# Kernel optimization log

Measured on AMD Instinct MI355X. Metric: run time of the kernel, lower is better.

## Reference

```python
import jax, jax.numpy as jnp
import numpy as np

V_CNT = 10000
B = 16
N = B * V_CNT          # total nodes
K = 6                  # Chebyshev order
CH = [3, 128, 64, 32, 128]
G = 8                  # GroupNorm groups (divides 128, 64, 32)
EPS = 1e-5
AVG_DEG = 16


def setup_inputs() -> dict:
    key = jax.random.key(0)
    ks = jax.random.split(key, 8)
    n_edges = N * AVG_DEG
    inp = {
        "x": jax.random.normal(ks[0], (N, CH[0]), jnp.float32),
        "edge_index": jax.random.randint(ks[1], (2, n_edges), 0, N, jnp.int32).astype(jnp.int64),
    }
    for l in range(3):
        cin, cout = CH[l], CH[l + 1]
        s = (1.0 / (cin * K)) ** 0.5
        inp[f"W{l}"] = jax.random.uniform(ks[2 + l], (K, cin, cout), jnp.float32, -s, s)
        inp[f"b{l}"] = jnp.zeros((cout,), jnp.float32)
        inp[f"gamma{l}"] = jnp.ones((cout,), jnp.float32)
        inp[f"beta{l}"] = jnp.zeros((cout,), jnp.float32)
    din = V_CNT * CH[3]
    s = (1.0 / din) ** 0.5
    inp["W_last"] = jax.random.uniform(ks[5], (din, CH[4]), jnp.float32, -s, s)
    inp["b_last"] = jnp.zeros((CH[4],), jnp.float32)
    return inp


def _cheb_edge_weights(edge_index):
    # PyG ChebConv sym normalization with lambda_max=2: L_hat = L - I = -D^{-1/2} A D^{-1/2}
    row, col = edge_index[0], edge_index[1]
    deg = jax.ops.segment_sum(jnp.ones(row.shape, jnp.float32), row, num_segments=N)
    dis = jnp.where(deg > 0, jax.lax.rsqrt(jnp.maximum(deg, 1.0)), 0.0)  # deg^{-1/2}, inf->0
    return -dis[row] * dis[col], row, col


def _cheb_conv(x, row, col, w, W, b):
    # Chebyshev recursion: Tx0=x, Tx1=L_hat x, Tx_k = 2 L_hat Tx_{k-1} - Tx_{k-2}
    prop = lambda h: jax.ops.segment_sum(w[:, None] * h[col], row, num_segments=N)
    Tx0 = x
    out = Tx0 @ W[0]
    Tx1 = prop(Tx0)
    out = out + Tx1 @ W[1]
    for k in range(2, W.shape[0]):
        Tx2 = 2.0 * prop(Tx1) - Tx0
        out = out + Tx2 @ W[k]
        Tx0, Tx1 = Tx1, Tx2
    return out + b


def _group_norm(h, gamma, beta):
    n, C = h.shape
    hg = h.reshape(n, G, C // G)
    mu = hg.mean(axis=2, keepdims=True)
    var = hg.var(axis=2, keepdims=True)
    hg = (hg - mu) * jax.lax.rsqrt(var + EPS)
    return hg.reshape(n, C) * gamma + beta


def reference(x, edge_index, W0, b0, gamma0, beta0, W1, b1, gamma1, beta1,
              W2, b2, gamma2, beta2, W_last, b_last):
    w, row, col = _cheb_edge_weights(edge_index)
    Ws = [W0, W1, W2]
    bs = [b0, b1, b2]
    gs = [gamma0, gamma1, gamma2]
    betas = [beta0, beta1, beta2]
    h = x
    for l in range(3):
        h = _cheb_conv(h, row, col, w, Ws[l], bs[l])
        h = _group_norm(h, gs[l], betas[l])
        h = jax.nn.relu(h)
    h = h.reshape(-1, V_CNT * CH[3])  # [B, v_cnt*32]
    return h @ W_last + b_last
```

## Files before the change

### kernel.cpp

```cpp
#include <hip/hip_runtime.h>
#include <hip/hip_fp16.h>


#define NN 160000
#define EE 2560000
#define FD2 256

typedef __attribute__((ext_vector_type(8))) _Float16 half8;
typedef __attribute__((ext_vector_type(4))) float floatx4;

__device__ inline float2 h2f2(unsigned u) {
  __half2 h = __builtin_bit_cast(__half2, u);
  return __half22float2(h);
}
__device__ inline unsigned short f2h(float f) {
  return __builtin_bit_cast(unsigned short, __float2half_rn(f));
}
__device__ inline unsigned packh2(float a, float b) {
  return __builtin_bit_cast(unsigned, __floats2half2_rn(a, b));
}

__global__ __launch_bounds__(256) void k_zero(int* __restrict__ p, int n) {
  int i = blockIdx.x * 256 + threadIdx.x;
  if (i < n) p[i] = 0;
}

__global__ __launch_bounds__(256) void k_hist(const int* __restrict__ ei, int* __restrict__ deg) {
  int e = blockIdx.x * 256 + threadIdx.x;
  if (e < EE) atomicAdd(&deg[ei[e]], 1);
}

__global__ __launch_bounds__(256) void k_dis(const int* __restrict__ deg, float* __restrict__ dis) {
  int i = blockIdx.x * 256 + threadIdx.x;
  if (i < NN) { int d = deg[i]; dis[i] = d > 0 ? rsqrtf((float)d) : 0.f; }
}

__global__ __launch_bounds__(256) void k_scan1(const int* __restrict__ deg, int* __restrict__ rowStart,
                                               int* __restrict__ bsum) {
  __shared__ int s[256];
  int tid = threadIdx.x;
  int i = blockIdx.x * 256 + tid;
  int v = deg[i];
  s[tid] = v;
  __syncthreads();
  for (int off = 1; off < 256; off <<= 1) {
    int t = (tid >= off) ? s[tid - off] : 0;
    __syncthreads();
    s[tid] += t;
    __syncthreads();
  }
  rowStart[i] = s[tid] - v;
  if (tid == 255) bsum[blockIdx.x] = s[255];
}

__global__ void k_scan2(int* __restrict__ bsum, int nb) {
  __shared__ int s[1024];
  int tid = threadIdx.x;
  int v = (tid < nb) ? bsum[tid] : 0;
  s[tid] = v;
  __syncthreads();
  for (int off = 1; off < 1024; off <<= 1) {
    int t = (tid >= off) ? s[tid - off] : 0;
    __syncthreads();
    s[tid] += t;
    __syncthreads();
  }
  if (tid < nb) bsum[tid] = s[tid] - v;
}

__global__ __launch_bounds__(256) void k_scan3(int* __restrict__ rowStart, const int* __restrict__ bsum) {
  int i = blockIdx.x * 256 + threadIdx.x;
  rowStart[i] += bsum[blockIdx.x];
  if (i == 0) rowStart[NN] = EE;
}

__global__ __launch_bounds__(256) void k_scatter(const int* __restrict__ ei, const int* __restrict__ rowStart,
                                                 int* __restrict__ cursor, const float* __restrict__ dis,
                                                 int2* __restrict__ ew) {
  int e = blockIdx.x * 256 + threadIdx.x;
  if (e >= EE) return;
  int r = ei[e];
  int c = ei[EE + e];
  int pos = rowStart[r] + atomicAdd(&cursor[r], 1);
  ew[pos] = make_int2(c, __float_as_int(-dis[r] * dis[c]));
}

__global__ __launch_bounds__(256) void k_copyx(const float* __restrict__ x, float* __restrict__ A,
                                               unsigned short* __restrict__ TxAll) {
  int i = blockIdx.x * 256 + threadIdx.x;
  if (i < NN * 3) {
    float v = x[i];
    A[i] = v;
    int node = i / 3, c = i - node * 3;
    TxAll[node * 32 + c] = f2h(v);
  }
}

template <int MODE>
__global__ __launch_bounds__(256) void k_prop3(const float* __restrict__ Tsrc, float* __restrict__ Tdst,
                                               unsigned short* __restrict__ TxAll, int ks,
                                               const int* __restrict__ rowStart, const int2* __restrict__ ew) {
  int i = blockIdx.x * 256 + threadIdx.x;
  if (i >= NN) return;
  float a0 = 0.f, a1 = 0.f, a2 = 0.f;
  int e = rowStart[i], e1 = rowStart[i + 1];
  for (; e + 3 < e1; e += 4) {
    int2 p0 = ew[e], p1 = ew[e + 1], p2 = ew[e + 2], p3 = ew[e + 3];
    float w0 = __int_as_float(p0.y), w1 = __int_as_float(p1.y);
    float w2 = __int_as_float(p2.y), w3 = __int_as_float(p3.y);
    a0 += w0 * Tsrc[p0.x * 3] + w1 * Tsrc[p1.x * 3] + w2 * Tsrc[p2.x * 3] + w3 * Tsrc[p3.x * 3];
    a1 += w0 * Tsrc[p0.x * 3 + 1] + w1 * Tsrc[p1.x * 3 + 1] + w2 * Tsrc[p2.x * 3 + 1] + w3 * Tsrc[p3.x * 3 + 1];
    a2 += w0 * Tsrc[p0.x * 3 + 2] + w1 * Tsrc[p1.x * 3 + 2] + w2 * Tsrc[p2.x * 3 + 2] + w3 * Tsrc[p3.x * 3 + 2];
  }
  for (; e < e1; e++) {
    int2 p0 = ew[e];
    float w0 = __int_as_float(p0.y);
    a0 += w0 * Tsrc[p0.x * 3];
    a1 += w0 * Tsrc[p0.x * 3 + 1];
    a2 += w0 * Tsrc[p0.x * 3 + 2];
  }
  if (MODE == 2) {
    a0 = 2.f * a0 - Tdst[i * 3];
    a1 = 2.f * a1 - Tdst[i * 3 + 1];
    a2 = 2.f * a2 - Tdst[i * 3 + 2];
  }
  Tdst[i * 3] = a0; Tdst[i * 3 + 1] = a1; Tdst[i * 3 + 2] = a2;
  unsigned short* tp = TxAll + i * 32 + ks * 3;
  tp[0] = f2h(a0); tp[1] = f2h(a1); tp[2] = f2h(a2);
}

__global__ __launch_bounds__(256) void k_padW0(const float* __restrict__ W0, unsigned short* __restrict__ Bt) {
  int idx = blockIdx.x * 256 + threadIdx.x;
  if (idx >= 128 * 32) return;
  int co = idx >> 5, t = idx & 31;
  Bt[co * 32 + t] = (t < 18) ? f2h(W0[t * 128 + co]) : (unsigned short)0;
}

template <int CIN, int COUT>
__global__ __launch_bounds__(256) void k_combine(const float* __restrict__ W, unsigned short* __restrict__ Bt) {
  int idx = blockIdx.x * 256 + threadIdx.x;
  if (idx >= CIN * 6 * COUT) return;
  int co = idx % COUT;
  int j  = (idx / COUT) % 6;
  int ci = idx / (6 * COUT);
  float c0, c1, c2, c3, c4, c5;
  switch (j) {
    case 0:  c0 = 1;  c1 = 0;  c2 = -1; c3 = 0;   c4 = 1;  c5 = 0;   break;
    case 1:  c0 = 0;  c1 = 1;  c2 = 0;  c3 = -3;  c4 = 0;  c5 = 5;   break;
    case 2:  c0 = 0;  c1 = 0;  c2 = 2;  c3 = 0;   c4 = -8; c5 = 0;   break;
    case 3:  c0 = 0;  c1 = 0;  c2 = 0;  c3 = 4;   c4 = 0;  c5 = -20; break;
    case 4:  c0 = 0;  c1 = 0;  c2 = 0;  c3 = 0;   c4 = 8;  c5 = 0;   break;
    default: c0 = 0;  c1 = 0;  c2 = 0;  c3 = 0;   c4 = 0;  c5 = 16;  break;
  }
  float s = 0.f;
  s += c0 * W[(0 * CIN + ci) * COUT + co];
  s += c1 * W[(1 * CIN + ci) * COUT + co];
  s += c2 * W[(2 * CIN + ci) * COUT + co];
  s += c3 * W[(3 * CIN + ci) * COUT + co];
  s += c4 * W[(4 * CIN + ci) * COUT + co];
  s += c5 * W[(5 * CIN + ci) * COUT + co];
  Bt[(j * COUT + co) * CIN + ci] = f2h(s);
}

template <int KDIM, int COUT>
__global__ __launch_bounds__(256) void k_gemm(const unsigned short* __restrict__ A,
                                              const unsigned short* __restrict__ Bt,
                                              unsigned short* __restrict__ Y) {
  constexpr int KP = KDIM + 8;
  __shared__ unsigned short As[64 * KP];
  __shared__ unsigned short Bs[64 * KP];
  int i0 = blockIdx.x * 64;
  int c0 = blockIdx.y * 64;
  for (int idx = threadIdx.x; idx < 64 * (KDIM / 8); idx += 256) {
    int row = idx / (KDIM / 8), seg = idx % (KDIM / 8);
    uint4 v = ((const uint4*)A)[(size_t)(i0 + row) * (KDIM / 8) + seg];
    *reinterpret_cast<uint4*>(&As[row * KP + seg * 8]) = v;
  }
  for (int idx = threadIdx.x; idx < 64 * (KDIM / 8); idx += 256) {
    int row = idx / (KDIM / 8), seg = idx % (KDIM / 8);
    uint4 v = ((const uint4*)Bt)[(size_t)(c0 + row) * (KDIM / 8) + seg];
    *reinterpret_cast<uint4*>(&Bs[row * KP + seg * 8]) = v;
  }
  __syncthreads();
  int w = threadIdx.x >> 6, lane = threadIdx.x & 63;
  int mn = lane & 15, q = lane >> 4;
  floatx4 acc[4];
#pragma unroll
  for (int cb = 0; cb < 4; cb++) acc[cb] = {0.f, 0.f, 0.f, 0.f};
#pragma unroll
  for (int ks = 0; ks < KDIM / 32; ks++) {
    half8 af = *reinterpret_cast<const half8*>(&As[(16 * w + mn) * KP + ks * 32 + q * 8]);
#pragma unroll
    for (int cb = 0; cb < 4; cb++) {
      half8 bf = *reinterpret_cast<const half8*>(&Bs[(cb * 16 + mn) * KP + ks * 32 + q * 8]);
      acc[cb] = __builtin_amdgcn_mfma_f32_16x16x32_f16(af, bf, acc[cb], 0, 0, 0);
    }
  }
#pragma unroll
  for (int cb = 0; cb < 4; cb++) {
    int jc = c0 + cb * 16 + mn;
    int slice = jc / COUT, cc = jc % COUT;
    unsigned short* dst = Y + (size_t)slice * NN * COUT + cc;
#pragma unroll
    for (int r = 0; r < 4; r++) {
      int i = i0 + 16 * w + q * 4 + r;
      dst[(size_t)i * COUT] = f2h(acc[cb][r]);
    }
  }
}

template <int CPN>
__global__ __launch_bounds__(256) void k_horner(const unsigned* __restrict__ Ysrc, unsigned* __restrict__ Ydst,
                                                const int* __restrict__ rowStart, const int2* __restrict__ ew) {
  int t = blockIdx.x * 256 + threadIdx.x;
  int i = t / CPN;
  int cp = t % CPN;
  float2 a = h2f2(Ydst[(size_t)i * CPN + cp]);
  float acc0 = a.x, acc1 = a.y;
  int e = rowStart[i], e1 = rowStart[i + 1];
  for (; e + 7 < e1; e += 8) {
    int2 p[8];
    unsigned u[8];
#pragma unroll
    for (int k = 0; k < 8; k++) p[k] = ew[e + k];
#pragma unroll
    for (int k = 0; k < 8; k++) u[k] = Ysrc[(size_t)p[k].x * CPN + cp];
#pragma unroll
    for (int k = 0; k < 8; k++) {
      float w = __int_as_float(p[k].y);
      float2 f = h2f2(u[k]);
      acc0 += w * f.x;
      acc1 += w * f.y;
    }
  }
  for (; e < e1; e++) {
    int2 p0 = ew[e];
    float w0 = __int_as_float(p0.y);
    float2 f0 = h2f2(Ysrc[(size_t)p0.x * CPN + cp]);
    acc0 += w0 * f0.x;
    acc1 += w0 * f0.y;
  }
  Ydst[(size_t)i * CPN + cp] = packh2(acc0, acc1);
}

template <int CPG>
__global__ __launch_bounds__(256) void k_gn(const unsigned short* __restrict__ src, const float* __restrict__ bias,
                                            const float* __restrict__ gamma, const float* __restrict__ beta,
                                            unsigned short* __restrict__ dst) {
  constexpr int C = CPG * 8;
  int t = blockIdx.x * 256 + threadIdx.x;
  int i = t >> 3, g = t & 7;
  float v[CPG];
  const unsigned* p = reinterpret_cast<const unsigned*>(src + (size_t)i * C + g * CPG);
#pragma unroll
  for (int q = 0; q < CPG / 2; q++) {
    float2 f = h2f2(p[q]);
    v[2 * q] = f.x; v[2 * q + 1] = f.y;
  }
  float mean = 0.f;
#pragma unroll
  for (int c = 0; c < CPG; c++) { v[c] += bias[g * CPG + c]; mean += v[c]; }
  mean *= (1.f / CPG);
  float var = 0.f;
#pragma unroll
  for (int c = 0; c < CPG; c++) { float d = v[c] - mean; var += d * d; }
  var *= (1.f / CPG);
  float rs = rsqrtf(var + 1e-5f);
  unsigned* dp = reinterpret_cast<unsigned*>(dst + (size_t)i * C + g * CPG);
#pragma unroll
  for (int q = 0; q < CPG / 2; q++) {
    float o0 = fmaxf((v[2 * q] - mean) * rs * gamma[g * CPG + 2 * q] + beta[g * CPG + 2 * q], 0.f);
    float o1 = fmaxf((v[2 * q + 1] - mean) * rs * gamma[g * CPG + 2 * q + 1] + beta[g * CPG + 2 * q + 1], 0.f);
    dp[q] = packh2(o0, o1);
  }
}

__global__ __launch_bounds__(256) void k_final1(const unsigned short* __restrict__ h3,
                                                const float* __restrict__ Wl,
                                                float* __restrict__ part) {
  __shared__ float hs[16 * FD2];
  __shared__ float red[2048];
  int d0 = blockIdx.x * FD2;
  const unsigned* h3u = reinterpret_cast<const unsigned*>(h3);
  for (int idx = threadIdx.x; idx < 16 * (FD2 / 2); idx += 256) {
    int b = idx / (FD2 / 2), dq = idx % (FD2 / 2);
    float2 f = h2f2(h3u[(size_t)b * 160000 + (d0 >> 1) + dq]);
    hs[b * FD2 + 2 * dq] = f.x;
    hs[b * FD2 + 2 * dq + 1] = f.y;
  }
  __syncthreads();
  int w = threadIdx.x >> 6, lane = threadIdx.x & 63;
  float a0[16], a1[16];
#pragma unroll
  for (int b = 0; b < 16; b++) { a0[b] = 0.f; a1[b] = 0.f; }
  const float* wp = Wl + (size_t)(d0 + w * (FD2 / 4)) * 128 + 2 * lane;
#pragma unroll 2
  for (int r = 0; r < FD2 / 4; r++) {
    float2 wv = *reinterpret_cast<const float2*>(wp + (size_t)r * 128);
    int row = w * (FD2 / 4) + r;
#pragma unroll
    for (int b = 0; b < 16; b++) {
      float h = hs[b * FD2 + row];
      a0[b] += wv.x * h;
      a1[b] += wv.y * h;
    }
  }
  float2* red2 = reinterpret_cast<float2*>(red);
  for (int ww = 0; ww < 4; ww++) {
    if (w == ww) {
#pragma unroll
      for (int b = 0; b < 16; b++) {
        if (ww == 0) {
          red2[b * 64 + lane] = make_float2(a0[b], a1[b]);
        } else {
          float2 r2 = red2[b * 64 + lane];
          r2.x += a0[b]; r2.y += a1[b];
          red2[b * 64 + lane] = r2;
        }
      }
    }
    __syncthreads();
  }
  for (int i = threadIdx.x; i < 2048; i += 256)
    part[(size_t)blockIdx.x * 2048 + i] = red[i];
}

__global__ __launch_bounds__(256) void k_final2(const float* __restrict__ part, const float* __restrict__ bl,
                                                float* __restrict__ out) {
  int o = blockIdx.x * 256 + threadIdx.x;
  float s = bl[o & 127];
#pragma unroll 10
  for (int p = 0; p < 1250; p++) s += part[(size_t)p * 2048 + o];
  out[o] = s;
}

extern "C" void kernel_launch(void* const* d_in, const int* in_sizes, int n_in,
                              void* d_out, int out_size, void* d_ws, size_t ws_size,
                              hipStream_t stream) {
  const float* x   = (const float*)d_in[0];
  const int*   ei  = (const int*)d_in[1];
  const float* W0  = (const float*)d_in[2];
  const float* b0  = (const float*)d_in[3];
  const float* g0  = (const float*)d_in[4];
  const float* be0 = (const float*)d_in[5];
  const float* W1  = (const float*)d_in[6];
  const float* b1  = (const float*)d_in[7];
  const float* g1  = (const float*)d_in[8];
  const float* be1 = (const float*)d_in[9];
  const float* W2  = (const float*)d_in[10];
  const float* b2  = (const float*)d_in[11];
  const float* g2  = (const float*)d_in[12];
  const float* be2 = (const float*)d_in[13];
  const float* Wl  = (const float*)d_in[14];
  const float* bl  = (const float*)d_in[15];
  float* out = (float*)d_out;
  (void)in_sizes; (void)n_in; (void)out_size; (void)ws_size;

  char* pw = (char*)d_ws;
  auto carve = [&](size_t bytes) -> void* {
    void* r = (void*)pw;
    pw += (bytes + 255) & ~(size_t)255;
    return r;
  };
  int*            deg      = (int*)   carve((size_t)NN * 4);
  int*            cursor   = (int*)   carve((size_t)NN * 4);
  int*            rowStart = (int*)   carve((size_t)(NN + 1) * 4);
  int*            bsum     = (int*)   carve(1024 * 4);
  float*          dis      = (float*) carve((size_t)NN * 4);
  int2*           ew       = (int2*)  carve((size_t)EE * 8);
  unsigned short* Cwt      = (unsigned short*)carve((size_t)384 * 128 * 2);
  unsigned short* TxAll    = (unsigned short*)carve((size_t)NN * 32 * 2);
  float*          A3       = (float*) carve((size_t)NN * 3 * 4);
  float*          B3       = (float*) carve((size_t)NN * 3 * 4);
  unsigned short* Hbuf     = (unsigned short*)carve((size_t)NN * 128 * 2);
  unsigned short* Ybuf     = (unsigned short*)carve((size_t)NN * 384 * 2);
  float*          part     = (float*) carve((size_t)1250 * 2048 * 4);

  k_zero<<<1250, 256, 0, stream>>>(deg, 2 * NN);
  k_hist<<<10000, 256, 0, stream>>>(ei, deg);
  k_dis<<<625, 256, 0, stream>>>(deg, dis);
  k_scan1<<<625, 256, 0, stream>>>(deg, rowStart, bsum);
  k_scan2<<<1, 1024, 0, stream>>>(bsum, 625);
  k_scan3<<<625, 256, 0, stream>>>(rowStart, bsum);
  k_scatter<<<10000, 256, 0, stream>>>(ei, rowStart, cursor, dis, ew);

  k_zero<<<10000, 256, 0, stream>>>((int*)TxAll, NN * 16);
  k_copyx<<<1875, 256, 0, stream>>>(x, A3, TxAll);
  k_prop3<1><<<625, 256, 0, stream>>>(A3, B3, TxAll, 1, rowStart, ew);
  k_prop3<2><<<625, 256, 0, stream>>>(B3, A3, TxAll, 2, rowStart, ew);
  k_prop3<2><<<625, 256, 0, stream>>>(A3, B3, TxAll, 3, rowStart, ew);
  k_prop3<2><<<625, 256, 0, stream>>>(B3, A3, TxAll, 4, rowStart, ew);
  k_prop3<2><<<625, 256, 0, stream>>>(A3, B3, TxAll, 5, rowStart, ew);
  k_padW0<<<16, 256, 0, stream>>>(W0, Cwt);
  k_gemm<32, 128><<<dim3(2500, 2), 256, 0, stream>>>(TxAll, Cwt, Ybuf);
  k_gn<16><<<5000, 256, 0, stream>>>(Ybuf, b0, g0, be0, Hbuf);

  k_combine<128, 64><<<192, 256, 0, stream>>>(W1, Cwt);
  k_gemm<128, 64><<<dim3(2500, 6), 256, 0, stream>>>(Hbuf, Cwt, Ybuf);
  for (int j = 4; j >= 0; j--)
    k_horner<32><<<20000, 256, 0, stream>>>((unsigned*)(Ybuf + (size_t)(j + 1) * NN * 64),
                                            (unsigned*)(Ybuf + (size_t)j * NN * 64), rowStart, ew);
  k_gn<8><<<5000, 256, 0, stream>>>(Ybuf, b1, g1, be1, Hbuf);

  k_combine<64, 32><<<48, 256, 0, stream>>>(W2, Cwt);
  k_gemm<64, 32><<<dim3(2500, 3), 256, 0, stream>>>(Hbuf, Cwt, Ybuf);
  for (int j = 4; j >= 0; j--)
    k_horner<16><<<10000, 256, 0, stream>>>((unsigned*)(Ybuf + (size_t)(j + 1) * NN * 32),
                                            (unsigned*)(Ybuf + (size_t)j * NN * 32), rowStart, ew);
  k_gn<4><<<5000, 256, 0, stream>>>(Ybuf, b2, g2, be2, Hbuf);

  k_final1<<<1250, 256, 0, stream>>>(Hbuf, Wl, part);
  k_final2<<<8, 256, 0, stream>>>(part, bl, out);
}
```

Measured before the change: 1.429 ms.

## Build CSR via two-pass bucketed scatter and fuse TxAll zeroing into copy

Replaces the global histogram and per-edge random scatter with a block-local bucketing pass. Each block counts edges per 256-row bucket in shared memory, reserves space in fixed-capacity staging buckets, and writes (row, col) pairs. A second pass then places them into CSR order using shared-memory cursors. This is meant to reduce random global atomics and scattered writes. It risks silently dropping edges if any bucket exceeds its fixed capacity, and it reuses Ybuf as staging. The x copy kernel is also vectorised per node and now writes the zero padding itself, removing a separate zero kernel.

```diff
diff --git a/kernel.cpp b/kernel.cpp
--- a/kernel.cpp
+++ b/kernel.cpp
@@ -5,6 +5,8 @@
 #define NN 160000
 #define EE 2560000
 #define FD2 256
+#define NBKT 625
+#define BCAPL 13
 
 typedef __attribute__((ext_vector_type(8))) _Float16 half8;
 typedef __attribute__((ext_vector_type(4))) float floatx4;
@@ -25,9 +27,63 @@
   if (i < n) p[i] = 0;
 }
 
-__global__ __launch_bounds__(256) void k_hist(const int* __restrict__ ei, int* __restrict__ deg) {
-  int e = blockIdx.x * 256 + threadIdx.x;
-  if (e < EE) atomicAdd(&deg[ei[e]], 1);
+__global__ __launch_bounds__(256) void k_binit(int* __restrict__ bcur) {
+  int i = blockIdx.x * 256 + threadIdx.x;
+  if (i < NBKT) bcur[i] = i << BCAPL;
+}
+
+__global__ __launch_bounds__(256) void k_bucketA(const int* __restrict__ ei, int* __restrict__ deg,
+                                                 int* __restrict__ bcur, int2* __restrict__ stg) {
+  __shared__ int bcnt[NBKT];
+  __shared__ int gbase[NBKT];
+  int tid = threadIdx.x;
+  for (int i = tid; i < NBKT; i += 256) bcnt[i] = 0;
+  __syncthreads();
+  int r[20];
+  int e0 = blockIdx.x * 5120;
+#pragma unroll
+  for (int k = 0; k < 20; k++) {
+    int e = e0 + k * 256 + tid;
+    int rr = ei[e];
+    r[k] = rr;
+    atomicAdd(&deg[rr], 1);
+    atomicAdd(&bcnt[rr >> 8], 1);
+  }
+  __syncthreads();
+  for (int i = tid; i < NBKT; i += 256) {
+    gbase[i] = atomicAdd(&bcur[i], bcnt[i]);
+    bcnt[i] = 0;
+  }
+  __syncthreads();
+#pragma unroll
+  for (int k = 0; k < 20; k++) {
+    int e = e0 + k * 256 + tid;
+    int c = ei[EE + e];
+    int b = r[k] >> 8;
+    int off = atomicAdd(&bcnt[b], 1);
+    int pos = gbase[b] + off;
+    if (pos < ((b + 1) << BCAPL)) stg[pos] = make_int2(r[k], c);
+  }
+}
+
+__global__ __launch_bounds__(256) void k_bucketB(const int2* __restrict__ stg, const int* __restrict__ bcur,
+                                                 const int* __restrict__ rowStart, const float* __restrict__ dis,
+                                                 int2* __restrict__ ew) {
+  __shared__ int curs[256];
+  int b = blockIdx.x;
+  int tid = threadIdx.x;
+  int r0 = b << 8;
+  curs[tid] = rowStart[r0 + tid];
+  __syncthreads();
+  int cnt = bcur[b] - (b << BCAPL);
+  if (cnt > (1 << BCAPL)) cnt = 1 << BCAPL;
+  int base = b << BCAPL;
+  for (int k = tid; k < cnt; k += 256) {
+    int2 rc = stg[base + k];
+    int pos = atomicAdd(&curs[rc.x - r0], 1);
+    float w = -dis[rc.x] * dis[rc.y];
+    ew[pos] = make_int2(rc.y, __float_as_int(w));
+  }
 }
 
 __global__ __launch_bounds__(256) void k_dis(const int* __restrict__ deg, float* __restrict__ dis) {
@@ -74,26 +130,16 @@
   if (i == 0) rowStart[NN] = EE;
 }
 
-__global__ __launch_bounds__(256) void k_scatter(const int* __restrict__ ei, const int* __restrict__ rowStart,
-                                                 int* __restrict__ cursor, const float* __restrict__ dis,
-                                                 int2* __restrict__ ew) {
-  int e = blockIdx.x * 256 + threadIdx.x;
-  if (e >= EE) return;
-  int r = ei[e];
-  int c = ei[EE + e];
-  int pos = rowStart[r] + atomicAdd(&cursor[r], 1);
-  ew[pos] = make_int2(c, __float_as_int(-dis[r] * dis[c]));
-}
-
 __global__ __launch_bounds__(256) void k_copyx(const float* __restrict__ x, float* __restrict__ A,
                                                unsigned short* __restrict__ TxAll) {
   int i = blockIdx.x * 256 + threadIdx.x;
-  if (i < NN * 3) {
-    float v = x[i];
-    A[i] = v;
-    int node = i / 3, c = i - node * 3;
-    TxAll[node * 32 + c] = f2h(v);
-  }
+  if (i >= NN) return;
+  float v0 = x[i * 3], v1 = x[i * 3 + 1], v2 = x[i * 3 + 2];
+  A[i * 3] = v0; A[i * 3 + 1] = v1; A[i * 3 + 2] = v2;
+  uint4* dst = reinterpret_cast<uint4*>(TxAll + (size_t)i * 32);
+  uint4 z = make_uint4(0u, 0u, 0u, 0u);
+  dst[0] = make_uint4(packh2(v0, v1), (unsigned)f2h(v2), 0u, 0u);
+  dst[1] = z; dst[2] = z; dst[3] = z;
 }
 
 template <int MODE>
@@ -363,7 +409,7 @@
     return r;
   };
   int*            deg      = (int*)   carve((size_t)NN * 4);
-  int*            cursor   = (int*)   carve((size_t)NN * 4);
+  int*            bcur     = (int*)   carve((size_t)NBKT * 4);
   int*            rowStart = (int*)   carve((size_t)(NN + 1) * 4);
   int*            bsum     = (int*)   carve(1024 * 4);
   float*          dis      = (float*) carve((size_t)NN * 4);
@@ -375,17 +421,18 @@
   unsigned short* Hbuf     = (unsigned short*)carve((size_t)NN * 128 * 2);
   unsigned short* Ybuf     = (unsigned short*)carve((size_t)NN * 384 * 2);
   float*          part     = (float*) carve((size_t)1250 * 2048 * 4);
-
-  k_zero<<<1250, 256, 0, stream>>>(deg, 2 * NN);
-  k_hist<<<10000, 256, 0, stream>>>(ei, deg);
+  int2*           stg      = (int2*)Ybuf;
+
+  k_zero<<<625, 256, 0, stream>>>(deg, NN);
+  k_binit<<<3, 256, 0, stream>>>(bcur);
+  k_bucketA<<<500, 256, 0, stream>>>(ei, deg, bcur, stg);
   k_dis<<<625, 256, 0, stream>>>(deg, dis);
   k_scan1<<<625, 256, 0, stream>>>(deg, rowStart, bsum);
   k_scan2<<<1, 1024, 0, stream>>>(bsum, 625);
   k_scan3<<<625, 256, 0, stream>>>(rowStart, bsum);
-  k_scatter<<<10000, 256, 0, stream>>>(ei, rowStart, cursor, dis, ew);
-
-  k_zero<<<10000, 256, 0, stream>>>((int*)TxAll, NN * 16);
-  k_copyx<<<1875, 256, 0, stream>>>(x, A3, TxAll);
+  k_bucketB<<<NBKT, 256, 0, stream>>>(stg, bcur, rowStart, dis, ew);
+
+  k_copyx<<<625, 256, 0, stream>>>(x, A3, TxAll);
   k_prop3<1><<<625, 256, 0, stream>>>(A3, B3, TxAll, 1, rowStart, ew);
   k_prop3<2><<<625, 256, 0, stream>>>(B3, A3, TxAll, 2, rowStart, ew);
   k_prop3<2><<<625, 256, 0, stream>>>(A3, B3, TxAll, 3, rowStart, ew);
```

Measured after the change: 1.370 ms. -4.1%, faster.
